# Optimization experiments

Measured on AMD Instinct MI355X. Metric: run time of the kernel, lower is better.

## Reference

```python
import jax, jax.numpy as jnp
import numpy as np

CNN_DIM = 256
CLASS_NUM = 6
NHOPS = 2
ATT_DIM = 50


def conv1d(x, w, b, pad):
    # x: [B, Cin, L], w: [Cout, Cin, K]
    y = jax.lax.conv_general_dilated(x, w, (1,), [(pad, pad)],
                                     dimension_numbers=('NCH', 'OIH', 'NCH'))
    return y + b[None, :, None]


def setup_inputs() -> dict:
    key = jax.random.key(0)
    ks = jax.random.split(key, 16)
    B, L, V, GE, DE = 8, 128, 30000, 300, 100
    IN = GE + DE
    C = CLASS_NUM
    s = 0.02
    inp = {}
    inp['x'] = jax.random.randint(ks[0], (B, L), 0, V)
    inp['x_len'] = L  # python int, stands in for x_len[0] (max length)
    inp['x_mask'] = jnp.ones((B, L), dtype=jnp.float32)
    inp['gen_table'] = jax.random.normal(ks[1], (V, GE), jnp.float32) * s
    inp['domain_table'] = jax.random.normal(ks[2], (V, DE), jnp.float32) * s
    inp['w1'] = jax.random.normal(ks[3], (128, IN, 5)) * s
    inp['b1'] = jnp.zeros((128,))
    inp['w2'] = jax.random.normal(ks[4], (128, IN, 3)) * s
    inp['b2'] = jnp.zeros((128,))
    inp['w3'] = jax.random.normal(ks[5], (256, 256, 5)) * s
    inp['b3'] = jnp.zeros((256,))
    inp['w4'] = jax.random.normal(ks[6], (256, 256, 5)) * s
    inp['b4'] = jnp.zeros((256,))
    inp['w5'] = jax.random.normal(ks[7], (256, 256, 5)) * s
    inp['b5'] = jnp.zeros((256,))
    inp['wq'] = jax.random.normal(ks[8], (CNN_DIM, ATT_DIM)) * s
    inp['bq'] = jnp.zeros((ATT_DIM,))
    inp['wv'] = jax.random.normal(ks[9], (CNN_DIM, ATT_DIM)) * s
    inp['bv'] = jnp.zeros((ATT_DIM,))
    inp['vv'] = jax.random.normal(ks[10], (ATT_DIM,)) * s
    inp['wf'] = jax.random.normal(ks[11], (2 * CNN_DIM + 3 * C, 2 * CNN_DIM)) * s
    inp['bf'] = jnp.zeros((2 * CNN_DIM,))
    inp['wc'] = jax.random.normal(ks[12], (2 * CNN_DIM, C)) * s
    inp['bc'] = jnp.zeros((C,))
    return inp


def reference(x, x_len, x_mask, gen_table, domain_table,
              w1, b1, w2, b2, w3, b3, w4, b4, w5, b5,
              wq, bq, wv, bv, vv, wf, bf, wc, bc):
    # embeddings (dropout omitted: eval mode)
    emb = jnp.concatenate([gen_table[x], domain_table[x]], axis=2)  # [B,L,400]
    xe = jnp.swapaxes(emb, 1, 2)  # [B,400,L]
    xc = jax.nn.relu(jnp.concatenate([conv1d(xe, w1, b1, 2),
                                      conv1d(xe, w2, b2, 1)], axis=1))
    xc = jax.nn.relu(conv1d(xc, w3, b3, 2))
    xc = jax.nn.relu(conv1d(xc, w4, b4, 2))
    xc = jax.nn.relu(conv1d(xc, w5, b5, 2))
    xc = jnp.swapaxes(xc, 1, 2)[:, :x_len, :]  # [B,L,256]
    mask = x_mask[:, :x_len]
    # perceptron (additive) self-attention: v^T tanh(Wq q_i + Wv v_j)
    q = xc @ wq + bq  # [B,L,50]
    v = xc @ wv + bv  # [B,L,50]
    scores = jnp.tanh(q[:, :, None, :] + v[:, None, :, :]) @ vv  # [B,L,L]
    scores = jnp.where(mask[:, None, :] == 0, -1e9, scores)
    attn = jax.nn.softmax(scores, axis=2)
    merged = jnp.einsum('bij,bjd->bid', attn, xc) * mask[:, :, None]
    xc = xc + merged
    B, L, D = xc.shape
    # grid features: (i,j) -> [h_i, h_j]
    features = jnp.concatenate([
        jnp.broadcast_to(xc[:, :, None, :], (B, L, L, D)),
        jnp.broadcast_to(xc[:, None, :, :], (B, L, L, D))], axis=3)  # [B,L,L,512]
    # upper-triangular validity mask on the grid
    m2 = jnp.triu(mask[:, None, :] * mask[:, :, None])[..., None]  # [B,L,L,1]
    logits = features @ wc + bc  # [B,L,L,C]
    for _ in range(NHOPS):
        probs = logits
        lg = probs * m2
        lm = jnp.maximum(jnp.max(lg, axis=1), jnp.max(lg, axis=2))  # [B,L,C]
        row = jnp.broadcast_to(lm[:, :, None, :], (B, L, L, lm.shape[-1]))
        grid = jnp.concatenate([row, jnp.swapaxes(row, 1, 2)], axis=3)  # [B,L,L,2C]
        features = jnp.concatenate([features, grid, probs], axis=3) @ wf + bf
        logits = features @ wc + bc
    return logits
```

## Files before the change

kernel.cpp:

```cpp
#include <hip/hip_runtime.h>
#include <hip/hip_bf16.h>
#include <math.h>

#define LSEQ 128
#define BB 8
#define M_TOK (BB*LSEQ)

struct PreArgs {
    const float* src[5];
    float* dst[5];
    int OC[5], CI[5], K[5];
    const int* x;
    const float4* gen4;
    const float4* dom4;
    float4* emb4;
};
__global__ __launch_bounds__(256) void stage_kernel(PreArgs a) {
    int y = blockIdx.y;
    if (y < 5) {
        int idx = blockIdx.x * 256 + threadIdx.x;
        int OC = a.OC[y], CI = a.CI[y], K = a.K[y];
        int total = OC * CI * K;
        if (idx >= total) return;
        int k = idx % K;
        int r = idx / K;
        int ci = r % CI;
        int oc = r / CI;
        a.dst[y][(ci * K + k) * OC + oc] = a.src[y][idx];
    } else {
        int m = blockIdx.x;
        if (m >= M_TOK) return;
        int t = a.x[m];
        int i = threadIdx.x;
        if (i < 100) {
            float4 v = (i < 75) ? a.gen4[t * 75 + i] : a.dom4[t * 25 + (i - 75)];
            a.emb4[m * 100 + i] = v;
        }
    }
}

__global__ __launch_bounds__(256) void conv1_v2(const float* __restrict__ emb,
        const float* __restrict__ w1T, const float* __restrict__ b1,
        const float* __restrict__ w2T, const float* __restrict__ b2,
        float* __restrict__ out) {
    __shared__ float xs[400 * 20];
    int pt = blockIdx.x;
    int b = pt >> 3;
    int l0 = (pt & 7) << 4;
    int ot = blockIdx.y;
    int tid = threadIdx.x;
    for (int idx = tid; idx < 400 * 20; idx += 256) {
        int p = idx / 400;
        int ci = idx - p * 400;
        int l = l0 - 2 + p;
        float v = 0.f;
        if (l >= 0 && l < LSEQ) v = emb[(b * LSEQ + l) * 400 + ci];
        xs[ci * 20 + p] = v;
    }
    __syncthreads();
    int o = tid & 31;
    int s = tid >> 5;
    float acc[16];
    #pragma unroll
    for (int p = 0; p < 16; ++p) acc[p] = 0.f;
    if (ot < 4) {
        const float* wp = w1T + (s * 50 * 5) * 128 + ot * 32 + o;
        for (int i = 0; i < 50; ++i) {
            const float4* x4 = (const float4*)(xs + (s * 50 + i) * 20);
            float4 A0 = x4[0], A1 = x4[1], A2 = x4[2], A3 = x4[3], A4 = x4[4];
            float xv[20] = {A0.x,A0.y,A0.z,A0.w, A1.x,A1.y,A1.z,A1.w,
                            A2.x,A2.y,A2.z,A2.w, A3.x,A3.y,A3.z,A3.w,
                            A4.x,A4.y,A4.z,A4.w};
            #pragma unroll
            for (int k = 0; k < 5; ++k) {
                float w = wp[k * 128];
                #pragma unroll
                for (int p = 0; p < 16; ++p) acc[p] += w * xv[p + k];
            }
            wp += 640;
        }
    } else {
        const float* wp = w2T + (s * 50 * 3) * 128 + (ot - 4) * 32 + o;
        for (int i = 0; i < 50; ++i) {
            const float4* x4 = (const float4*)(xs + (s * 50 + i) * 20);
            float4 A0 = x4[0], A1 = x4[1], A2 = x4[2], A3 = x4[3], A4 = x4[4];
            float xv[20] = {A0.x,A0.y,A0.z,A0.w, A1.x,A1.y,A1.z,A1.w,
                            A2.x,A2.y,A2.z,A2.w, A3.x,A3.y,A3.z,A3.w,
                            A4.x,A4.y,A4.z,A4.w};
            #pragma unroll
            for (int k = 0; k < 3; ++k) {
                float w = wp[k * 128];
                #pragma unroll
                for (int p = 0; p < 16; ++p) acc[p] += w * xv[p + k + 1];
            }
            wp += 384;
        }
    }
    __syncthreads();
    float* rs = xs;
    #pragma unroll
    for (int p = 0; p < 16; ++p) rs[s * 512 + p * 32 + o] = acc[p];
    __syncthreads();
    #pragma unroll
    for (int r = 0; r < 2; ++r) {
        int idx = r * 256 + tid;
        int p = idx >> 5, oo = idx & 31;
        float sum = 0.f;
        #pragma unroll
        for (int ss = 0; ss < 8; ++ss) sum += rs[ss * 512 + p * 32 + oo];
        float bs = (ot < 4) ? b1[ot * 32 + oo] : b2[(ot - 4) * 32 + oo];
        out[(b * LSEQ + l0 + p) * 256 + ot * 32 + oo] = fmaxf(sum + bs, 0.f);
    }
}

__global__ __launch_bounds__(256) void conv256_v2(const float* __restrict__ in,
        const float* __restrict__ wT, const float* __restrict__ bias,
        float* __restrict__ out) {
    __shared__ float xs[256 * 20];
    int pt = blockIdx.x;
    int b = pt >> 3;
    int l0 = (pt & 7) << 4;
    int ot = blockIdx.y;
    int tid = threadIdx.x;
    for (int idx = tid; idx < 256 * 20; idx += 256) {
        int p = idx >> 8;
        int ci = idx & 255;
        int l = l0 - 2 + p;
        float v = 0.f;
        if (l >= 0 && l < LSEQ) v = in[(b * LSEQ + l) * 256 + ci];
        xs[ci * 20 + p] = v;
    }
    __syncthreads();
    int o = tid & 31;
    int s = tid >> 5;
    int oc0 = ot * 32;
    float acc[16];
    #pragma unroll
    for (int p = 0; p < 16; ++p) acc[p] = 0.f;
    const float* wp = wT + (s * 32 * 5) * 256 + oc0 + o;
    for (int i = 0; i < 32; ++i) {
        const float4* x4 = (const float4*)(xs + (s * 32 + i) * 20);
        float4 A0 = x4[0], A1 = x4[1], A2 = x4[2], A3 = x4[3], A4 = x4[4];
        float xv[20] = {A0.x,A0.y,A0.z,A0.w, A1.x,A1.y,A1.z,A1.w,
                        A2.x,A2.y,A2.z,A2.w, A3.x,A3.y,A3.z,A3.w,
                        A4.x,A4.y,A4.z,A4.w};
        #pragma unroll
        for (int k = 0; k < 5; ++k) {
            float w = wp[k * 256];
            #pragma unroll
            for (int p = 0; p < 16; ++p) acc[p] += w * xv[p + k];
        }
        wp += 1280;
    }
    __syncthreads();
    float* rs = xs;
    #pragma unroll
    for (int p = 0; p < 16; ++p) rs[s * 512 + p * 32 + o] = acc[p];
    __syncthreads();
    #pragma unroll
    for (int r = 0; r < 2; ++r) {
        int idx = r * 256 + tid;
        int p = idx >> 5, oo = idx & 31;
        float sum = 0.f;
        #pragma unroll
        for (int ss = 0; ss < 8; ++ss) sum += rs[ss * 512 + p * 32 + oo];
        out[(b * LSEQ + l0 + p) * 256 + oc0 + oo] = fmaxf(sum + bias[oc0 + oo], 0.f);
    }
}

__global__ __launch_bounds__(128) void qv_v2(const float* __restrict__ xc,
        const float* __restrict__ wq, const float* __restrict__ bq,
        const float* __restrict__ wv, const float* __restrict__ bv,
        float* __restrict__ q, float* __restrict__ v) {
    int m = blockIdx.x;
    int tid = threadIdx.x;
    int w = tid >> 6, d = tid & 63;
    if (d >= 50) return;
    const float* W = w ? wv : wq;
    float a = w ? bv[d] : bq[d];
    const float* xm = xc + m * 256;
    #pragma unroll 8
    for (int c = 0; c < 256; ++c) a += xm[c] * W[c * 50 + d];
    (w ? v : q)[m * 50 + d] = a;
}

__global__ __launch_bounds__(256) void attn_v2(const float* __restrict__ xc,
        const float* __restrict__ q, const float* __restrict__ v,
        const float* __restrict__ vv, const float* __restrict__ xmask,
        const float* __restrict__ wc, const float* __restrict__ bc,
        float* __restrict__ xc2, float* __restrict__ f0, float* __restrict__ g0) {
    __shared__ float vs[128 * 50];
    __shared__ float spart[128], aarr[128], xrow[256], qrow[52], vvs[52], red[4];
    int bi = blockIdx.x;
    int b = bi >> 7;
    int tid = threadIdx.x;
    for (int idx = tid; idx < 128 * 50; idx += 256) vs[idx] = v[b * 6400 + idx];
    if (tid < 50) { qrow[tid] = q[bi * 50 + tid]; vvs[tid] = vv[tid]; }
    __syncthreads();
    int j = tid & 127, half = tid >> 7;
    int d0 = half * 25;
    const float* vj = vs + j * 50 + d0;
    float s = 0.f;
    #pragma unroll
    for (int d = 0; d < 25; ++d) {
        float x = qrow[d0 + d] + vj[d];
        float e = __expf(2.f * x);
        s += (1.f - 2.f / (e + 1.f)) * vvs[d0 + d];
    }
    if (half) spart[j] = s;
    __syncthreads();
    float stot = 0.f;
    if (!half) {
        stot = s + spart[j];
        if (xmask[b * LSEQ + j] == 0.f) stot = -1e9f;
    }
    if (tid < 128) {
        float m = stot;
        #pragma unroll
        for (int off = 32; off >= 1; off >>= 1) m = fmaxf(m, __shfl_xor(m, off, 64));
        if ((tid & 63) == 0) red[tid >> 6] = m;
    }
    __syncthreads();
    float mx = fmaxf(red[0], red[1]);
    float e = 0.f;
    if (tid < 128) {
        e = __expf(stot - mx);
        float su = e;
        #pragma unroll
        for (int off = 32; off >= 1; off >>= 1) su += __shfl_xor(su, off, 64);
        if ((tid & 63) == 0) red[2 + (tid >> 6)] = su;
    }
    __syncthreads();
    float denom = red[2] + red[3];
    if (tid < 128) aarr[j] = e / denom;
    __syncthreads();
    float maskI = xmask[bi];
    const float* xcb = xc + b * LSEQ * 256;
    float acc = 0.f;
    #pragma unroll 8
    for (int jj = 0; jj < 128; ++jj) acc += aarr[jj] * xcb[jj * 256 + tid];
    float val = xc[bi * 256 + tid] + acc * maskI;
    xc2[bi * 256 + tid] = val;
    xrow[tid] = val;
    __syncthreads();
    int grp = tid >> 4, l16 = tid & 15;
    if (grp < 12) {
        int c = grp % 6, gsel = grp / 6;
        const float* wcc = wc + gsel * 256 * 6 + c;
        float a = 0.f;
        #pragma unroll
        for (int ch = l16; ch < 256; ch += 16) a += xrow[ch] * wcc[ch * 6];
        #pragma unroll
        for (int off = 8; off >= 1; off >>= 1) a += __shfl_down(a, off, 16);
        if (l16 == 0) {
            if (gsel == 0) f0[bi * 6 + c] = a + bc[c];
            else           g0[bi * 6 + c] = a;
        }
    }
}

__global__ __launch_bounds__(64) void precomp1_kernel(const float* __restrict__ wf,
        const float* __restrict__ wc, float* __restrict__ Wfc) {
    int r = blockIdx.x;
    int tid = threadIdx.x;
    float p[6] = {0,0,0,0,0,0};
    const float* row = wf + r * 512;
    for (int n = tid; n < 512; n += 64) {
        float a = row[n];
        #pragma unroll
        for (int c = 0; c < 6; ++c) p[c] += a * wc[n * 6 + c];
    }
    #pragma unroll
    for (int c = 0; c < 6; ++c)
        for (int off = 32; off >= 1; off >>= 1) p[c] += __shfl_xor(p[c], off, 64);
    if (tid == 0) {
        #pragma unroll
        for (int c = 0; c < 6; ++c) Wfc[r * 6 + c] = p[c];
    }
}

__global__ __launch_bounds__(64) void precomp2_kernel(const float* __restrict__ wf,
        const float* __restrict__ bf, const float* __restrict__ wc,
        const float* __restrict__ Wfc, float* __restrict__ U) {
    int r = blockIdx.x;
    int tid = threadIdx.x;
    const float* row = (r < 530) ? (wf + r * 512) : bf;
    float p[12];
    #pragma unroll
    for (int c = 0; c < 12; ++c) p[c] = 0.f;
    for (int n = tid; n < 512; n += 64) {
        float a = row[n];
        #pragma unroll
        for (int c = 0; c < 6; ++c) {
            p[c]     += a * wc[n * 6 + c];
            p[c + 6] += a * Wfc[n * 6 + c];
        }
    }
    #pragma unroll
    for (int c = 0; c < 12; ++c)
        for (int off = 32; off >= 1; off >>= 1) p[c] += __shfl_xor(p[c], off, 64);
    if (tid == 0) {
        #pragma unroll
        for (int c = 0; c < 12; ++c) U[r * 12 + c] = p[c];
    }
}

__global__ __launch_bounds__(128) void lm_scan_v3(const float* __restrict__ f,
        const float* __restrict__ g, int stride, float* __restrict__ lm) {
    __shared__ float sf[128], sg[128];
    int bc = blockIdx.x;
    int b = bc / 6, c = bc - b * 6;
    int p = threadIdx.x;
    float fv = f[(b * LSEQ + p) * stride + c];
    float gv = g[(b * LSEQ + p) * stride + c];
    sf[p] = fv; sg[p] = gv;
    __syncthreads();
    float pf = fv, sgx = gv;
    #pragma unroll
    for (int off = 1; off < 128; off <<= 1) {
        float a = (p >= off) ? sf[p - off] : -INFINITY;
        float d = (p + off < 128) ? sg[p + off] : -INFINITY;
        __syncthreads();
        pf = fmaxf(pf, a); sgx = fmaxf(sgx, d);
        sf[p] = pf; sg[p] = sgx;
        __syncthreads();
    }
    float M1 = pf + gv;
    if (p < LSEQ - 1) M1 = fmaxf(M1, 0.f);
    float M2 = fv + sgx;
    if (p > 0) M2 = fmaxf(M2, 0.f);
    lm[(b * LSEQ + p) * 6 + c] = fmaxf(M1, M2);
}

__global__ __launch_bounds__(64) void hopfold_kernel(const float* __restrict__ xc2,
        const float* __restrict__ U, const float* __restrict__ lm0,
        const float* __restrict__ f0, const float* __restrict__ g0,
        const float* __restrict__ bc,
        float* __restrict__ outF, float* __restrict__ outG) {
    int m = blockIdx.x;
    int y = blockIdx.y;
    int tid = threadIdx.x;
    const float* Urows = U + (y ? 256 : 0) * 12;
    float p[12];
    #pragma unroll
    for (int c = 0; c < 12; ++c) p[c] = 0.f;
    for (int k = tid; k < 256; k += 64) {
        float a = xc2[m * 256 + k];
        const float* ur = Urows + k * 12;
        #pragma unroll
        for (int c = 0; c < 12; ++c) p[c] += a * ur[c];
    }
    #pragma unroll
    for (int c = 0; c < 12; ++c)
        for (int off = 32; off >= 1; off >>= 1) p[c] += __shfl_xor(p[c], off, 64);
    if (tid == 0) {
        const float* Bb = U + (y ? 518 : 512) * 12;
        const float* Db = U + 524 * 12;
        const float* fg = y ? g0 : f0;
        float* out = y ? outG : outF;
        float lmv[6], fgv[6];
        #pragma unroll
        for (int j = 0; j < 6; ++j) { lmv[j] = lm0[m * 6 + j]; fgv[j] = fg[m * 6 + j]; }
        #pragma unroll
        for (int c = 0; c < 12; ++c) {
            float s = p[c];
            #pragma unroll
            for (int j = 0; j < 6; ++j) s += lmv[j] * Bb[j * 12 + c] + fgv[j] * Db[j * 12 + c];
            if (!y) { s += U[530 * 12 + c]; if (c < 6) s += bc[c]; }
            out[m * 12 + c] = s;
        }
    }
}

__global__ __launch_bounds__(128) void f2g2_kernel(const float* __restrict__ f1phi,
        const float* __restrict__ g1gam, const float* __restrict__ lm1,
        const float* __restrict__ U, const float* __restrict__ bc,
        float* __restrict__ f2, float* __restrict__ g2) {
    __shared__ float Us[19 * 12], bcs[6];
    int tid = threadIdx.x;
    for (int i = tid; i < 19 * 12; i += 128) Us[i] = U[512 * 12 + i];
    if (tid < 6) bcs[tid] = bc[tid];
    __syncthreads();
    int m = blockIdx.x * 128 + tid;
    float lmv[6], f1v[6], g1v[6];
    #pragma unroll
    for (int j = 0; j < 6; ++j) {
        lmv[j] = lm1[m * 6 + j];
        f1v[j] = f1phi[m * 12 + j];
        g1v[j] = g1gam[m * 12 + j];
    }
    #pragma unroll
    for (int c = 0; c < 6; ++c) {
        float sf = f1phi[m * 12 + 6 + c] + Us[18 * 12 + c] + bcs[c];
        float sg = g1gam[m * 12 + 6 + c];
        #pragma unroll
        for (int j = 0; j < 6; ++j) {
            sf += lmv[j] * Us[j * 12 + c]       + f1v[j] * Us[(12 + j) * 12 + c];
            sg += lmv[j] * Us[(6 + j) * 12 + c] + g1v[j] * Us[(12 + j) * 12 + c];
        }
        f2[m * 6 + c] = sf;
        g2[m * 6 + c] = sg;
    }
}

__global__ __launch_bounds__(256) void writeout_kernel(const float* __restrict__ f2,
        const float* __restrict__ g2, float* __restrict__ out) {
    int idx = blockIdx.x * 256 + threadIdx.x;
    int c = idx % 6;
    int r = idx / 6;
    int j = r & 127;
    int bi = r >> 7;
    int b = bi >> 7;
    out[idx] = f2[bi * 6 + c] + g2[(b * LSEQ + j) * 6 + c];
}

extern "C" void kernel_launch(void* const* d_in, const int* in_sizes, int n_in,
                              void* d_out, int out_size, void* d_ws, size_t ws_size,
                              hipStream_t stream) {
    const int*   x     = (const int*)d_in[0];
    const float* xmask = (const float*)d_in[2];
    const float* gen   = (const float*)d_in[3];
    const float* dom   = (const float*)d_in[4];
    const float* w1    = (const float*)d_in[5];
    const float* b1    = (const float*)d_in[6];
    const float* w2    = (const float*)d_in[7];
    const float* b2    = (const float*)d_in[8];
    const float* w3    = (const float*)d_in[9];
    const float* b3    = (const float*)d_in[10];
    const float* w4    = (const float*)d_in[11];
    const float* b4    = (const float*)d_in[12];
    const float* w5    = (const float*)d_in[13];
    const float* b5    = (const float*)d_in[14];
    const float* wq    = (const float*)d_in[15];
    const float* bq    = (const float*)d_in[16];
    const float* wv    = (const float*)d_in[17];
    const float* bv    = (const float*)d_in[18];
    const float* vv    = (const float*)d_in[19];
    const float* wf    = (const float*)d_in[20];
    const float* bf    = (const float*)d_in[21];
    const float* wc    = (const float*)d_in[22];
    const float* bc    = (const float*)d_in[23];

    float* ws = (float*)d_ws;
    float* emb   = ws;
    float* bufA  = emb   + 409600;
    float* bufB  = bufA  + 262144;
    float* xc2   = bufB  + 262144;
    float* qb    = xc2   + 262144;
    float* vb    = qb    + 51200;
    float* w1T   = vb    + 51200;
    float* w2T   = w1T   + 256000;
    float* w3T   = w2T   + 153600;
    float* w4T   = w3T   + 327680;
    float* w5T   = w4T   + 327680;
    float* Wfc   = w5T   + 327680;
    float* U     = Wfc   + 3072;
    float* f0    = U     + 6372;
    float* g0    = f0    + 6144;
    float* lm0   = g0    + 6144;
    float* lm1   = lm0   + 6144;
    float* f1phi = lm1   + 6144;
    float* g1gam = f1phi + 12288;
    float* f2    = g1gam + 12288;
    float* g2    = f2    + 6144;

    precomp1_kernel<<<512, 64, 0, stream>>>(wf, wc, Wfc);
    precomp2_kernel<<<531, 64, 0, stream>>>(wf, bf, wc, Wfc, U);

    PreArgs pa;
    pa.src[0] = w1;  pa.dst[0] = w1T; pa.OC[0] = 128; pa.CI[0] = 400; pa.K[0] = 5;
    pa.src[1] = w2;  pa.dst[1] = w2T; pa.OC[1] = 128; pa.CI[1] = 400; pa.K[1] = 3;
    pa.src[2] = w3;  pa.dst[2] = w3T; pa.OC[2] = 256; pa.CI[2] = 256; pa.K[2] = 5;
    pa.src[3] = w4;  pa.dst[3] = w4T; pa.OC[3] = 256; pa.CI[3] = 256; pa.K[3] = 5;
    pa.src[4] = w5;  pa.dst[4] = w5T; pa.OC[4] = 256; pa.CI[4] = 256; pa.K[4] = 5;
    pa.x = x; pa.gen4 = (const float4*)gen; pa.dom4 = (const float4*)dom;
    pa.emb4 = (float4*)emb;
    stage_kernel<<<dim3(1280, 6), 256, 0, stream>>>(pa);

    conv1_v2<<<dim3(64, 8), 256, 0, stream>>>(emb, w1T, b1, w2T, b2, bufA);
    conv256_v2<<<dim3(64, 8), 256, 0, stream>>>(bufA, w3T, b3, bufB);
    conv256_v2<<<dim3(64, 8), 256, 0, stream>>>(bufB, w4T, b4, bufA);
    conv256_v2<<<dim3(64, 8), 256, 0, stream>>>(bufA, w5T, b5, bufB);

    qv_v2<<<M_TOK, 128, 0, stream>>>(bufB, wq, bq, wv, bv, qb, vb);
    attn_v2<<<M_TOK, 256, 0, stream>>>(bufB, qb, vb, vv, xmask, wc, bc, xc2, f0, g0);

    lm_scan_v3<<<48, 128, 0, stream>>>(f0, g0, 6, lm0);
    hopfold_kernel<<<dim3(M_TOK, 2), 64, 0, stream>>>(xc2, U, lm0, f0, g0, bc, f1phi, g1gam);
    lm_scan_v3<<<48, 128, 0, stream>>>(f1phi, g1gam, 12, lm1);
    f2g2_kernel<<<8, 128, 0, stream>>>(f1phi, g1gam, lm1, U, bc, f2, g2);

    writeout_kernel<<<(BB*LSEQ*LSEQ*6)/256, 256, 0, stream>>>(f2, g2, (float*)d_out);
}
```

Before: 270.3 us.

## Fuse weight precompute into staging/conv1 and merge hop tail into one kernel

Moves the Wfc precompute into an extra grid row of the staging kernel and the U precompute into an extra grid row of conv1, removing two launches. The lm scans, hop fold and f2/g2 kernels are replaced by one per-batch 1024-thread tail kernel that keeps U, scans and intermediates in shared memory and uses wave shuffles for the prefix max. This cuts launch overhead and global round trips, but the tail now runs on only 8 blocks, and conv1 blocks serially process up to 9 U rows.

```diff
diff --git a/kernel.cpp b/kernel.cpp
--- a/kernel.cpp
+++ b/kernel.cpp
@@ -14,6 +14,9 @@
     const float4* gen4;
     const float4* dom4;
     float4* emb4;
+    const float* wf;
+    const float* wc;
+    float* Wfc;
 };
 __global__ __launch_bounds__(256) void stage_kernel(PreArgs a) {
     int y = blockIdx.y;
@@ -27,7 +30,7 @@
         int ci = r % CI;
         int oc = r / CI;
         a.dst[y][(ci * K + k) * OC + oc] = a.src[y][idx];
-    } else {
+    } else if (y == 5) {
         int m = blockIdx.x;
         if (m >= M_TOK) return;
         int t = a.x[m];
@@ -36,18 +39,71 @@
             float4 v = (i < 75) ? a.gen4[t * 75 + i] : a.dom4[t * 25 + (i - 75)];
             a.emb4[m * 100 + i] = v;
         }
+    } else {
+        int r = blockIdx.x;
+        if (r >= 512 || threadIdx.x >= 64) return;
+        int l = threadIdx.x;
+        float p[6] = {0,0,0,0,0,0};
+        const float* row = a.wf + r * 512;
+        #pragma unroll
+        for (int k = 0; k < 8; ++k) {
+            int n = l + 64 * k;
+            float v = row[n];
+            #pragma unroll
+            for (int c = 0; c < 6; ++c) p[c] += v * a.wc[n * 6 + c];
+        }
+        #pragma unroll
+        for (int c = 0; c < 6; ++c)
+            for (int off = 32; off >= 1; off >>= 1) p[c] += __shfl_xor(p[c], off, 64);
+        if (l == 0) {
+            #pragma unroll
+            for (int c = 0; c < 6; ++c) a.Wfc[r * 6 + c] = p[c];
+        }
     }
 }
 
 __global__ __launch_bounds__(256) void conv1_v2(const float* __restrict__ emb,
         const float* __restrict__ w1T, const float* __restrict__ b1,
         const float* __restrict__ w2T, const float* __restrict__ b2,
-        float* __restrict__ out) {
+        float* __restrict__ out,
+        const float* __restrict__ wf, const float* __restrict__ bf,
+        const float* __restrict__ wc, const float* __restrict__ Wfc,
+        float* __restrict__ U) {
     __shared__ float xs[400 * 20];
+    int ot = blockIdx.y;
+    if (ot == 8) {
+        if (threadIdx.x >= 64) return;
+        int l = threadIdx.x;
+        for (int i = 0; i < 9; ++i) {
+            int r = blockIdx.x + 64 * i;
+            if (r >= 531) break;
+            const float* row = (r < 530) ? (wf + r * 512) : bf;
+            float p[12];
+            #pragma unroll
+            for (int c = 0; c < 12; ++c) p[c] = 0.f;
+            #pragma unroll
+            for (int k = 0; k < 8; ++k) {
+                int n = l + 64 * k;
+                float v = row[n];
+                #pragma unroll
+                for (int c = 0; c < 6; ++c) {
+                    p[c]     += v * wc[n * 6 + c];
+                    p[c + 6] += v * Wfc[n * 6 + c];
+                }
+            }
+            #pragma unroll
+            for (int c = 0; c < 12; ++c)
+                for (int off = 32; off >= 1; off >>= 1) p[c] += __shfl_xor(p[c], off, 64);
+            if (l == 0) {
+                #pragma unroll
+                for (int c = 0; c < 12; ++c) U[r * 12 + c] = p[c];
+            }
+        }
+        return;
+    }
     int pt = blockIdx.x;
     int b = pt >> 3;
     int l0 = (pt & 7) << 4;
-    int ot = blockIdx.y;
     int tid = threadIdx.x;
     for (int idx = tid; idx < 400 * 20; idx += 256) {
         int p = idx / 400;
@@ -259,147 +315,159 @@
     }
 }
 
-__global__ __launch_bounds__(64) void precomp1_kernel(const float* __restrict__ wf,
-        const float* __restrict__ wc, float* __restrict__ Wfc) {
-    int r = blockIdx.x;
+__global__ __launch_bounds__(1024) void tail_kernel(const float* __restrict__ xc2,
+        const float* __restrict__ U, const float* __restrict__ f0g,
+        const float* __restrict__ g0g, const float* __restrict__ bc,
+        float* __restrict__ f2, float* __restrict__ g2) {
+    __shared__ float Ul[531 * 12];
+    __shared__ float sf[768], sg[768];
+    __shared__ float pmax[768], smax[768];
+    __shared__ float lm[768];
+    __shared__ float fF[128 * 12], fG[128 * 12];
+    int b = blockIdx.x;
     int tid = threadIdx.x;
-    float p[6] = {0,0,0,0,0,0};
-    const float* row = wf + r * 512;
-    for (int n = tid; n < 512; n += 64) {
-        float a = row[n];
-        #pragma unroll
-        for (int c = 0; c < 6; ++c) p[c] += a * wc[n * 6 + c];
-    }
-    #pragma unroll
-    for (int c = 0; c < 6; ++c)
-        for (int off = 32; off >= 1; off >>= 1) p[c] += __shfl_xor(p[c], off, 64);
-    if (tid == 0) {
-        #pragma unroll
-        for (int c = 0; c < 6; ++c) Wfc[r * 6 + c] = p[c];
-    }
-}
-
-__global__ __launch_bounds__(64) void precomp2_kernel(const float* __restrict__ wf,
-        const float* __restrict__ bf, const float* __restrict__ wc,
-        const float* __restrict__ Wfc, float* __restrict__ U) {
-    int r = blockIdx.x;
-    int tid = threadIdx.x;
-    const float* row = (r < 530) ? (wf + r * 512) : bf;
-    float p[12];
-    #pragma unroll
-    for (int c = 0; c < 12; ++c) p[c] = 0.f;
-    for (int n = tid; n < 512; n += 64) {
-        float a = row[n];
-        #pragma unroll
-        for (int c = 0; c < 6; ++c) {
-            p[c]     += a * wc[n * 6 + c];
-            p[c + 6] += a * Wfc[n * 6 + c];
-        }
-    }
-    #pragma unroll
-    for (int c = 0; c < 12; ++c)
-        for (int off = 32; off >= 1; off >>= 1) p[c] += __shfl_xor(p[c], off, 64);
-    if (tid == 0) {
-        #pragma unroll
-        for (int c = 0; c < 12; ++c) U[r * 12 + c] = p[c];
-    }
-}
-
-__global__ __launch_bounds__(128) void lm_scan_v3(const float* __restrict__ f,
-        const float* __restrict__ g, int stride, float* __restrict__ lm) {
-    __shared__ float sf[128], sg[128];
-    int bc = blockIdx.x;
-    int b = bc / 6, c = bc - b * 6;
-    int p = threadIdx.x;
-    float fv = f[(b * LSEQ + p) * stride + c];
-    float gv = g[(b * LSEQ + p) * stride + c];
-    sf[p] = fv; sg[p] = gv;
-    __syncthreads();
-    float pf = fv, sgx = gv;
-    #pragma unroll
-    for (int off = 1; off < 128; off <<= 1) {
-        float a = (p >= off) ? sf[p - off] : -INFINITY;
-        float d = (p + off < 128) ? sg[p + off] : -INFINITY;
-        __syncthreads();
-        pf = fmaxf(pf, a); sgx = fmaxf(sgx, d);
-        sf[p] = pf; sg[p] = sgx;
-        __syncthreads();
-    }
-    float M1 = pf + gv;
-    if (p < LSEQ - 1) M1 = fmaxf(M1, 0.f);
-    float M2 = fv + sgx;
-    if (p > 0) M2 = fmaxf(M2, 0.f);
-    lm[(b * LSEQ + p) * 6 + c] = fmaxf(M1, M2);
-}
-
-__global__ __launch_bounds__(64) void hopfold_kernel(const float* __restrict__ xc2,
-        const float* __restrict__ U, const float* __restrict__ lm0,
-        const float* __restrict__ f0, const float* __restrict__ g0,
-        const float* __restrict__ bc,
-        float* __restrict__ outF, float* __restrict__ outG) {
-    int m = blockIdx.x;
-    int y = blockIdx.y;
-    int tid = threadIdx.x;
-    const float* Urows = U + (y ? 256 : 0) * 12;
-    float p[12];
-    #pragma unroll
-    for (int c = 0; c < 12; ++c) p[c] = 0.f;
-    for (int k = tid; k < 256; k += 64) {
-        float a = xc2[m * 256 + k];
-        const float* ur = Urows + k * 12;
-        #pragma unroll
-        for (int c = 0; c < 12; ++c) p[c] += a * ur[c];
-    }
-    #pragma unroll
-    for (int c = 0; c < 12; ++c)
-        for (int off = 32; off >= 1; off >>= 1) p[c] += __shfl_xor(p[c], off, 64);
-    if (tid == 0) {
-        const float* Bb = U + (y ? 518 : 512) * 12;
-        const float* Db = U + 524 * 12;
-        const float* fg = y ? g0 : f0;
-        float* out = y ? outG : outF;
-        float lmv[6], fgv[6];
-        #pragma unroll
-        for (int j = 0; j < 6; ++j) { lmv[j] = lm0[m * 6 + j]; fgv[j] = fg[m * 6 + j]; }
+    int w = tid >> 6, l = tid & 63;
+    for (int i = tid; i < 531 * 12; i += 1024) Ul[i] = U[i];
+    for (int i = tid; i < 768; i += 1024) {
+        int p = i / 6, c = i - p * 6;
+        sf[c * 128 + p] = f0g[b * 768 + i];
+        sg[c * 128 + p] = g0g[b * 768 + i];
+    }
+    __syncthreads();
+    if (w < 6) {
+        int c = w;
+        float v0 = sf[c * 128 + 2 * l], v1 = sf[c * 128 + 2 * l + 1];
+        float lo = fmaxf(v0, v1), sc = lo;
+        #pragma unroll
+        for (int off = 1; off < 64; off <<= 1) {
+            float o = __shfl_up(sc, off, 64);
+            if (l >= off) sc = fmaxf(sc, o);
+        }
+        float E = __shfl_up(sc, 1, 64); if (l == 0) E = -INFINITY;
+        pmax[c * 128 + 2 * l] = fmaxf(E, v0);
+        pmax[c * 128 + 2 * l + 1] = sc;
+    } else if (w < 12) {
+        int c = w - 6;
+        int i0 = 127 - 2 * l, i1 = 126 - 2 * l;
+        float v0 = sg[c * 128 + i0], v1 = sg[c * 128 + i1];
+        float lo = fmaxf(v0, v1), sc = lo;
+        #pragma unroll
+        for (int off = 1; off < 64; off <<= 1) {
+            float o = __shfl_up(sc, off, 64);
+            if (l >= off) sc = fmaxf(sc, o);
+        }
+        float E = __shfl_up(sc, 1, 64); if (l == 0) E = -INFINITY;
+        smax[c * 128 + i0] = fmaxf(E, v0);
+        smax[c * 128 + i1] = sc;
+    }
+    __syncthreads();
+    if (tid < 768) {
+        int p = tid / 6, c = tid - p * 6;
+        float M1 = pmax[c * 128 + p] + sg[c * 128 + p];
+        if (p < LSEQ - 1) M1 = fmaxf(M1, 0.f);
+        float M2 = sf[c * 128 + p] + smax[c * 128 + p];
+        if (p > 0) M2 = fmaxf(M2, 0.f);
+        lm[p * 6 + c] = fmaxf(M1, M2);
+    }
+    __syncthreads();
+    {
+        int t = tid >> 3, y = (tid >> 2) & 1, ks = tid & 3;
+        int ybase = y ? 256 : 0;
+        float acc[12];
+        #pragma unroll
+        for (int c = 0; c < 12; ++c) acc[c] = 0.f;
+        const float4* xr = (const float4*)(xc2 + (b * LSEQ + t) * 256 + ks * 64);
+        #pragma unroll 4
+        for (int kk = 0; kk < 16; ++kk) {
+            float4 x4 = xr[kk];
+            int kb = (ybase + ks * 64 + kk * 4) * 12;
+            #pragma unroll
+            for (int c = 0; c < 12; ++c) {
+                acc[c] += x4.x * Ul[kb + c] + x4.y * Ul[kb + 12 + c]
+                        + x4.z * Ul[kb + 24 + c] + x4.w * Ul[kb + 36 + c];
+            }
+        }
         #pragma unroll
         for (int c = 0; c < 12; ++c) {
-            float s = p[c];
-            #pragma unroll
-            for (int j = 0; j < 6; ++j) s += lmv[j] * Bb[j * 12 + c] + fgv[j] * Db[j * 12 + c];
-            if (!y) { s += U[530 * 12 + c]; if (c < 6) s += bc[c]; }
-            out[m * 12 + c] = s;
-        }
-    }
-}
-
-__global__ __launch_bounds__(128) void f2g2_kernel(const float* __restrict__ f1phi,
-        const float* __restrict__ g1gam, const float* __restrict__ lm1,
-        const float* __restrict__ U, const float* __restrict__ bc,
-        float* __restrict__ f2, float* __restrict__ g2) {
-    __shared__ float Us[19 * 12], bcs[6];
-    int tid = threadIdx.x;
-    for (int i = tid; i < 19 * 12; i += 128) Us[i] = U[512 * 12 + i];
-    if (tid < 6) bcs[tid] = bc[tid];
-    __syncthreads();
-    int m = blockIdx.x * 128 + tid;
-    float lmv[6], f1v[6], g1v[6];
-    #pragma unroll
-    for (int j = 0; j < 6; ++j) {
-        lmv[j] = lm1[m * 6 + j];
-        f1v[j] = f1phi[m * 12 + j];
-        g1v[j] = g1gam[m * 12 + j];
-    }
-    #pragma unroll
-    for (int c = 0; c < 6; ++c) {
-        float sf = f1phi[m * 12 + 6 + c] + Us[18 * 12 + c] + bcs[c];
-        float sg = g1gam[m * 12 + 6 + c];
-        #pragma unroll
-        for (int j = 0; j < 6; ++j) {
-            sf += lmv[j] * Us[j * 12 + c]       + f1v[j] * Us[(12 + j) * 12 + c];
-            sg += lmv[j] * Us[(6 + j) * 12 + c] + g1v[j] * Us[(12 + j) * 12 + c];
-        }
-        f2[m * 6 + c] = sf;
-        g2[m * 6 + c] = sg;
+            acc[c] += __shfl_down(acc[c], 1, 4);
+            acc[c] += __shfl_down(acc[c], 2, 4);
+        }
+        if (ks == 0) {
+            int Bb = (y ? 518 : 512) * 12;
+            int Db = 524 * 12;
+            float lmv[6], fgv[6];
+            #pragma unroll
+            for (int j2 = 0; j2 < 6; ++j2) {
+                lmv[j2] = lm[t * 6 + j2];
+                fgv[j2] = y ? sg[j2 * 128 + t] : sf[j2 * 128 + t];
+            }
+            float* dst = y ? (fG + t * 12) : (fF + t * 12);
+            #pragma unroll
+            for (int c = 0; c < 12; ++c) {
+                float s = acc[c];
+                #pragma unroll
+                for (int j2 = 0; j2 < 6; ++j2)
+                    s += lmv[j2] * Ul[Bb + j2 * 12 + c] + fgv[j2] * Ul[Db + j2 * 12 + c];
+                if (!y) { s += Ul[530 * 12 + c]; if (c < 6) s += bc[c]; }
+                dst[c] = s;
+            }
+        }
+    }
+    __syncthreads();
+    if (w < 6) {
+        int c = w;
+        float v0 = fF[(2 * l) * 12 + c], v1 = fF[(2 * l + 1) * 12 + c];
+        float lo = fmaxf(v0, v1), sc = lo;
+        #pragma unroll
+        for (int off = 1; off < 64; off <<= 1) {
+            float o = __shfl_up(sc, off, 64);
+            if (l >= off) sc = fmaxf(sc, o);
+        }
+        float E = __shfl_up(sc, 1, 64); if (l == 0) E = -INFINITY;
+        pmax[c * 128 + 2 * l] = fmaxf(E, v0);
+        pmax[c * 128 + 2 * l + 1] = sc;
+    } else if (w < 12) {
+        int c = w - 6;
+        int i0 = 127 - 2 * l, i1 = 126 - 2 * l;
+        float v0 = fG[i0 * 12 + c], v1 = fG[i1 * 12 + c];
+        float lo = fmaxf(v0, v1), sc = lo;
+        #pragma unroll
+        for (int off = 1; off < 64; off <<= 1) {
+            float o = __shfl_up(sc, off, 64);
+            if (l >= off) sc = fmaxf(sc, o);
+        }
+        float E = __shfl_up(sc, 1, 64); if (l == 0) E = -INFINITY;
+        smax[c * 128 + i0] = fmaxf(E, v0);
+        smax[c * 128 + i1] = sc;
+    }
+    __syncthreads();
+    if (tid < 768) {
+        int p = tid / 6, c = tid - p * 6;
+        float M1 = pmax[c * 128 + p] + fG[p * 12 + c];
+        if (p < LSEQ - 1) M1 = fmaxf(M1, 0.f);
+        float M2 = fF[p * 12 + c] + smax[c * 128 + p];
+        if (p > 0) M2 = fmaxf(M2, 0.f);
+        lm[p * 6 + c] = fmaxf(M1, M2);
+    }
+    __syncthreads();
+    if (tid < 768) {
+        int p = tid / 6, c = tid - p * 6;
+        float lmv[6], f1v[6], g1v[6];
+        #pragma unroll
+        for (int j2 = 0; j2 < 6; ++j2) {
+            lmv[j2] = lm[p * 6 + j2];
+            f1v[j2] = fF[p * 12 + j2];
+            g1v[j2] = fG[p * 12 + j2];
+        }
+        float sfv = fF[p * 12 + 6 + c] + Ul[530 * 12 + c] + bc[c];
+        float sgv = fG[p * 12 + 6 + c];
+        #pragma unroll
+        for (int j2 = 0; j2 < 6; ++j2) {
+            sfv += lmv[j2] * Ul[(512 + j2) * 12 + c] + f1v[j2] * Ul[(524 + j2) * 12 + c];
+            sgv += lmv[j2] * Ul[(518 + j2) * 12 + c] + g1v[j2] * Ul[(524 + j2) * 12 + c];
+        }
+        f2[b * 768 + tid] = sfv;
+        g2[b * 768 + tid] = sgv;
     }
 }
 
@@ -457,15 +525,8 @@
     float* U     = Wfc   + 3072;
     float* f0    = U     + 6372;
     float* g0    = f0    + 6144;
-    float* lm0   = g0    + 6144;
-    float* lm1   = lm0   + 6144;
-    float* f1phi = lm1   + 6144;
-    float* g1gam = f1phi + 12288;
-    float* f2    = g1gam + 12288;
+    float* f2    = g0    + 6144;
     float* g2    = f2    + 6144;
-
-    precomp1_kernel<<<512, 64, 0, stream>>>(wf, wc, Wfc);
-    precomp2_kernel<<<531, 64, 0, stream>>>(wf, bf, wc, Wfc, U);
 
     PreArgs pa;
     pa.src[0] = w1;  pa.dst[0] = w1T; pa.OC[0] = 128; pa.CI[0] = 400; pa.K[0] = 5;
@@ -475,9 +536,11 @@
     pa.src[4] = w5;  pa.dst[4] = w5T; pa.OC[4] = 256; pa.CI[4] = 256; pa.K[4] = 5;
     pa.x = x; pa.gen4 = (const float4*)gen; pa.dom4 = (const float4*)dom;
     pa.emb4 = (float4*)emb;
-    stage_kernel<<<dim3(1280, 6), 256, 0, stream>>>(pa);
-
-    conv1_v2<<<dim3(64, 8), 256, 0, stream>>>(emb, w1T, b1, w2T, b2, bufA);
+    pa.wf = wf; pa.wc = wc; pa.Wfc = Wfc;
+    stage_kernel<<<dim3(1280, 7), 256, 0, stream>>>(pa);
+
+    conv1_v2<<<dim3(64, 9), 256, 0, stream>>>(emb, w1T, b1, w2T, b2, bufA,
+                                              wf, bf, wc, Wfc, U);
     conv256_v2<<<dim3(64, 8), 256, 0, stream>>>(bufA, w3T, b3, bufB);
     conv256_v2<<<dim3(64, 8), 256, 0, stream>>>(bufB, w4T, b4, bufA);
     conv256_v2<<<dim3(64, 8), 256, 0, stream>>>(bufA, w5T, b5, bufB);
@@ -485,10 +548,7 @@
     qv_v2<<<M_TOK, 128, 0, stream>>>(bufB, wq, bq, wv, bv, qb, vb);
     attn_v2<<<M_TOK, 256, 0, stream>>>(bufB, qb, vb, vv, xmask, wc, bc, xc2, f0, g0);
 
-    lm_scan_v3<<<48, 128, 0, stream>>>(f0, g0, 6, lm0);
-    hopfold_kernel<<<dim3(M_TOK, 2), 64, 0, stream>>>(xc2, U, lm0, f0, g0, bc, f1phi, g1gam);
-    lm_scan_v3<<<48, 128, 0, stream>>>(f1phi, g1gam, 12, lm1);
-    f2g2_kernel<<<8, 128, 0, stream>>>(f1phi, g1gam, lm1, U, bc, f2, g2);
+    tail_kernel<<<BB, 1024, 0, stream>>>(xc2, U, f0, g0, bc, f2, g2);
 
     writeout_kernel<<<(BB*LSEQ*LSEQ*6)/256, 256, 0, stream>>>(f2, g2, (float*)d_out);
 }
```

After: 298.7 us. 1.11x slower.
